# Kernel optimization log

Measured on AMD Instinct MI355X. Metric: run time of the kernel, lower is better.

## Reference

```python
import jax, jax.numpy as jnp
import numpy as np

N, E, B, D, H, C = 50000, 800000, 128, 64, 128, 2
EPS = 1e-5


def setup_inputs() -> dict:
    key = jax.random.key(0)
    ks = jax.random.split(key, 12)
    s = 0.1
    return {
        "x": jax.random.normal(ks[0], (N, D), jnp.float32),
        "edge_index": jax.random.randint(ks[1], (2, E), 0, N, jnp.int64),
        "batch": jnp.sort(jax.random.randint(ks[2], (N,), 0, B, jnp.int64)),
        "W_l": jax.random.normal(ks[3], (D, D), jnp.float32) * s,
        "b_l": jnp.zeros((D,), jnp.float32),
        "W_r": jax.random.normal(ks[4], (D, D), jnp.float32) * s,
        "W_res": jax.random.normal(ks[5], (D, D), jnp.float32) * s,
        "b_res": jnp.zeros((D,), jnp.float32),
        "gamma": jnp.ones((D,), jnp.float32),
        "beta": jnp.zeros((D,), jnp.float32),
        "gate_W1": jax.random.normal(ks[6], (D, D), jnp.float32) * s,
        "gate_b1": jnp.zeros((D,), jnp.float32),
        "gate_W2": jax.random.normal(ks[7], (D, 1), jnp.float32) * s,
        "gate_b2": jnp.zeros((1,), jnp.float32),
        "W_p1": jax.random.normal(ks[8], (D, H), jnp.float32) * s,
        "b_p1": jnp.zeros((H,), jnp.float32),
        "W_p2": jax.random.normal(ks[9], (H, C), jnp.float32) * s,
        "b_p2": jnp.zeros((C,), jnp.float32),
    }


def reference(x, edge_index, batch, W_l, b_l, W_r, W_res, b_res, gamma, beta,
              gate_W1, gate_b1, gate_W2, gate_b2, W_p1, b_p1, W_p2, b_p2):
    src, dst = edge_index[0], edge_index[1]
    # SAGEConv, mean aggregation: gather source feats, scatter-mean to target
    agg = jax.ops.segment_sum(x[src], dst, num_segments=N)          # [N, D]
    cnt = jax.ops.segment_sum(jnp.ones((E,), x.dtype), dst, num_segments=N)
    mean = agg / jnp.maximum(cnt, 1.0)[:, None]
    h = mean @ W_l + b_l + x @ W_r                                   # [N, D]
    # dropout is identity (eval mode)
    # BatchNorm1d (training-mode math: biased batch stats)
    mu = jnp.mean(h, axis=0)
    var = jnp.var(h, axis=0)
    h = (h - mu) * jax.lax.rsqrt(var + EPS) * gamma + beta
    # residual projection of the original features
    h = h + x @ W_res + b_res
    # GlobalAttention pooling: per-graph softmax over gate scores
    gate = jax.nn.relu(h @ gate_W1 + gate_b1) @ gate_W2 + gate_b2    # [N, 1]
    g = gate[:, 0]
    gmax = jax.ops.segment_max(g, batch, num_segments=B)
    gmax = jnp.where(jnp.isfinite(gmax), gmax, 0.0)
    e = jnp.exp(g - gmax[batch])
    z = jax.ops.segment_sum(e, batch, num_segments=B)
    alpha = e / jnp.maximum(z, 1e-16)[batch]
    pooled = jax.ops.segment_sum(alpha[:, None] * h, batch, num_segments=B)  # [B, D]
    # 2-layer predictor MLP with ReLU between
    out = jax.nn.relu(pooled @ W_p1 + b_p1) @ W_p2 + b_p2            # [B, C]
    return out
```

## Files before the change

kernel.cpp:

```cpp
#include <hip/hip_runtime.h>
#include <math.h>

#define N_NODES 50000
#define N_EDGES 800000
#define BATCHES 128
#define DIM 64
#define HID 128
#define NCLS 2
#define EPSV 1e-5f
#define MAXD 64

#define NPART 8
#define PART_SZ ((N_NODES + NPART - 1) / NPART)
#define EPB 2048
#define NCHK_E ((N_EDGES + EPB - 1) / EPB)
#define NCHUNK1 782

typedef __attribute__((ext_vector_type(8))) short bf16x8;
typedef __attribute__((ext_vector_type(4))) float f32x4;

__device__ __forceinline__ unsigned short f2bf(float f){
  unsigned u = __float_as_uint(f);
  u += 0x7FFFu + ((u >> 16) & 1u);
  return (unsigned short)(u >> 16);
}
__device__ __forceinline__ float bf2f(unsigned short h){
  return __uint_as_float(((unsigned)h) << 16);
}
__device__ __forceinline__ void split2(float f, unsigned short& hi, unsigned short& lo){
  hi = f2bf(f);
  lo = f2bf(f - bf2f(hi));
}
__device__ __forceinline__ uint4 pack8(const unsigned short* s){
  uint4 u;
  u.x = (unsigned)s[0] | ((unsigned)s[1] << 16);
  u.y = (unsigned)s[2] | ((unsigned)s[3] << 16);
  u.z = (unsigned)s[4] | ((unsigned)s[5] << 16);
  u.w = (unsigned)s[6] | ((unsigned)s[7] << 16);
  return u;
}

__global__ void k_scatter(const int* __restrict__ ei, int* __restrict__ cnt,
                          unsigned short* __restrict__ csr){
  const int p = blockIdx.x & (NPART-1);
  const int c = blockIdx.x >> 3;
  const int lo = p * PART_SZ;
  const int hi = lo + PART_SZ;
  const int e0 = c * EPB;
  const int e1 = (e0 + EPB < N_EDGES) ? e0 + EPB : N_EDGES;
  for (int i = e0 + threadIdx.x; i < e1; i += 256){
    int d = ei[N_EDGES + i];
    if (d >= lo && d < hi){
      int s = ei[i];
      int pos = atomicAdd(&cnt[d], 1);
      csr[(size_t)d*MAXD + pos] = (unsigned short)s;
    }
  }
}

__global__ void k_mean(const float* __restrict__ x,
                       const unsigned short* __restrict__ csr,
                       const int* __restrict__ cnt, float* __restrict__ meanb){
  const int node = (blockIdx.x*256 + threadIdx.x) >> 6;
  const int lane = threadIdx.x & 63;
  const int g = lane >> 4, f = lane & 15;
  const int dg = cnt[node];
  const size_t start = (size_t)node * MAXD;
  float4 acc = make_float4(0.f,0.f,0.f,0.f);
  int e = (lane < dg) ? (int)csr[start + lane] : 0;
  int i = 0;
  for (; i + 16 <= dg; i += 16){
    int s0 = __shfl(e, i +      g, 64);
    int s1 = __shfl(e, i + 4  + g, 64);
    int s2 = __shfl(e, i + 8  + g, 64);
    int s3 = __shfl(e, i + 12 + g, 64);
    float4 v0 = *(const float4*)&x[(size_t)s0*DIM + f*4];
    float4 v1 = *(const float4*)&x[(size_t)s1*DIM + f*4];
    float4 v2 = *(const float4*)&x[(size_t)s2*DIM + f*4];
    float4 v3 = *(const float4*)&x[(size_t)s3*DIM + f*4];
    acc.x += v0.x + v1.x + v2.x + v3.x;
    acc.y += v0.y + v1.y + v2.y + v3.y;
    acc.z += v0.z + v1.z + v2.z + v3.z;
    acc.w += v0.w + v1.w + v2.w + v3.w;
  }
  for (; i < dg; i += 4){
    int idx = i + g;
    int srcl = (idx < dg) ? idx : (dg - 1);
    int s = __shfl(e, srcl, 64);
    if (idx < dg){
      float4 v = *(const float4*)&x[(size_t)s*DIM + f*4];
      acc.x += v.x; acc.y += v.y; acc.z += v.z; acc.w += v.w;
    }
  }
  acc.x += __shfl_xor(acc.x, 16, 64); acc.x += __shfl_xor(acc.x, 32, 64);
  acc.y += __shfl_xor(acc.y, 16, 64); acc.y += __shfl_xor(acc.y, 32, 64);
  acc.z += __shfl_xor(acc.z, 16, 64); acc.z += __shfl_xor(acc.z, 32, 64);
  acc.w += __shfl_xor(acc.w, 16, 64); acc.w += __shfl_xor(acc.w, 32, 64);
  if (g == 0){
    float inv = 1.f / fmaxf((float)dg, 1.f);
    float4 r = make_float4(acc.x*inv, acc.y*inv, acc.z*inv, acc.w*inv);
    *(float4*)&meanb[(size_t)node*DIM + f*4] = r;
  }
}

__global__ void __launch_bounds__(256) k_lin1(
    const float* __restrict__ meanb, const float* __restrict__ x,
    const float* __restrict__ Wl, const float* __restrict__ bl,
    const float* __restrict__ Wr, float* __restrict__ hbuf,
    float* __restrict__ pstat){
  __shared__ __align__(16) short sB[2][64][136];
  __shared__ __align__(16) short sA[2][64][72];
  const int tid  = threadIdx.x;
  const int lane = tid & 63, w = tid >> 6;
  const int jc   = lane & 15;
  const int mrow = 16*w + jc;
  const int koff = (lane >> 4) * 8;
  const int r0   = 16*w + (lane >> 4)*4;
  const int base = blockIdx.x * 64;

  {
    const int k0 = 32 * w;
    #pragma unroll
    for (int kc = 0; kc < 4; ++kc){
      unsigned short h[8], l[8];
      #pragma unroll
      for (int i = 0; i < 8; ++i){
        int k = k0 + 8*kc + i;
        float v = (k < 64) ? Wl[k*DIM + lane] : Wr[(k-64)*DIM + lane];
        split2(v, h[i], l[i]);
      }
      *(uint4*)&sB[0][lane][k0 + 8*kc] = pack8(h);
      *(uint4*)&sB[1][lane][k0 + 8*kc] = pack8(l);
    }
  }

  float blv[4];
  #pragma unroll
  for (int nt = 0; nt < 4; ++nt) blv[nt] = bl[nt*16 + jc];

  f32x4 acc[4] = {};
  #pragma unroll
  for (int half = 0; half < 2; ++half){
    const float* __restrict__ src = half ? x : meanb;
    __syncthreads();
    {
      const int row = tid >> 2;
      const int kq  = (tid & 3) * 16;
      const int node = base + row;
      #pragma unroll
      for (int cc = 0; cc < 4; ++cc){
        float4 v = make_float4(0.f,0.f,0.f,0.f);
        if (node < N_NODES) v = *(const float4*)&src[(size_t)node*DIM + kq + 4*cc];
        unsigned short h[4], l[4];
        split2(v.x,h[0],l[0]); split2(v.y,h[1],l[1]);
        split2(v.z,h[2],l[2]); split2(v.w,h[3],l[3]);
        uint2 ph, pl;
        ph.x = (unsigned)h[0] | ((unsigned)h[1]<<16);
        ph.y = (unsigned)h[2] | ((unsigned)h[3]<<16);
        pl.x = (unsigned)l[0] | ((unsigned)l[1]<<16);
        pl.y = (unsigned)l[2] | ((unsigned)l[3]<<16);
        *(uint2*)&sA[0][row][kq + 4*cc] = ph;
        *(uint2*)&sA[1][row][kq + 4*cc] = pl;
      }
    }
    __syncthreads();
    #pragma unroll
    for (int kt2 = 0; kt2 < 2; ++kt2){
      const int ka = kt2*32 + koff;
      const int kb = half*64 + ka;
      bf16x8 ah = *(const bf16x8*)&sA[0][mrow][ka];
      bf16x8 al = *(const bf16x8*)&sA[1][mrow][ka];
      #pragma unroll
      for (int nt = 0; nt < 4; ++nt){
        const int nr = nt*16 + jc;
        bf16x8 bh = *(const bf16x8*)&sB[0][nr][kb];
        bf16x8 bo = *(const bf16x8*)&sB[1][nr][kb];
        acc[nt] = __builtin_amdgcn_mfma_f32_16x16x32_bf16(ah, bh, acc[nt], 0,0,0);
        acc[nt] = __builtin_amdgcn_mfma_f32_16x16x32_bf16(al, bh, acc[nt], 0,0,0);
        acc[nt] = __builtin_amdgcn_mfma_f32_16x16x32_bf16(ah, bo, acc[nt], 0,0,0);
      }
    }
  }

  float s1[4] = {0.f,0.f,0.f,0.f}, s2[4] = {0.f,0.f,0.f,0.f};
  #pragma unroll
  for (int nt = 0; nt < 4; ++nt){
    const int col = nt*16 + jc;
    #pragma unroll
    for (int r = 0; r < 4; ++r){
      const int node = base + r0 + r;
      float v = acc[nt][r] + blv[nt];
      if (node < N_NODES){
        hbuf[(size_t)node*DIM + col] = v;
        s1[nt] += v; s2[nt] += v*v;
      }
    }
  }

  __syncthreads();
  float* sred = (float*)sA;
  #pragma unroll
  for (int nt = 0; nt < 4; ++nt){
    float a = s1[nt], b = s2[nt];
    a += __shfl_xor(a, 16, 64); a += __shfl_xor(a, 32, 64);
    b += __shfl_xor(b, 16, 64); b += __shfl_xor(b, 32, 64);
    if ((lane >> 4) == 0){
      sred[0*256 + w*64 + nt*16 + jc] = a;
      sred[1*256 + w*64 + nt*16 + jc] = b;
    }
  }
  __syncthreads();
  if (tid < 64){
    float a = sred[tid] + sred[64+tid] + sred[128+tid] + sred[192+tid];
    float b = sred[256+tid] + sred[320+tid] + sred[384+tid] + sred[448+tid];
    pstat[(size_t)blockIdx.x*128 + tid]      = a;
    pstat[(size_t)blockIdx.x*128 + 64 + tid] = b;
  }
}

__global__ void __launch_bounds__(256) k_stats(
    const float* __restrict__ pstat, float* __restrict__ muinv){
  __shared__ float r1[256], r2[256];
  const int j = blockIdx.x;
  const int t = threadIdx.x;
  float s1 = 0.f, s2 = 0.f;
  for (int c = t; c < NCHUNK1; c += 256){
    s1 += pstat[(size_t)c*128 + j];
    s2 += pstat[(size_t)c*128 + 64 + j];
  }
  r1[t] = s1; r2[t] = s2;
  __syncthreads();
  for (int st = 128; st > 0; st >>= 1){
    if (t < st){ r1[t] += r1[t+st]; r2[t] += r2[t+st]; }
    __syncthreads();
  }
  if (t == 0){
    float mu = r1[0] / (float)N_NODES;
    float var = r2[0] / (float)N_NODES - mu*mu;
    muinv[j] = mu;
    muinv[DIM+j] = 1.0f / sqrtf(var + EPSV);
  }
}

__device__ __forceinline__ void stage_w64(short* sWh, short* sWl_,
                                          const float* __restrict__ W,
                                          int w, int lane){
  const int k0 = 16 * w;
  #pragma unroll
  for (int kc = 0; kc < 2; ++kc){
    unsigned short h[8], l[8];
    #pragma unroll
    for (int i = 0; i < 8; ++i){
      int k = k0 + 8*kc + i;
      split2(W[k*DIM + lane], h[i], l[i]);
    }
    *(uint4*)&sWh[lane*72 + k0 + 8*kc] = pack8(h);
    *(uint4*)&sWl_[lane*72 + k0 + 8*kc] = pack8(l);
  }
}

__global__ void __launch_bounds__(256) k_lin2(
    const float* __restrict__ x, const float* __restrict__ hbuf,
    const float* __restrict__ Wres, const float* __restrict__ bres,
    const float* __restrict__ gamma, const float* __restrict__ beta,
    const float* __restrict__ muinv,
    const float* __restrict__ gW1, const float* __restrict__ gb1,
    const float* __restrict__ gW2, const float* __restrict__ gb2,
    const int* __restrict__ batch,
    float* __restrict__ zbuf, float* __restrict__ pooled){
  __shared__ __align__(16) short sW[2][64][72];
  __shared__ __align__(16) short sA[2][64][72];
  __shared__ int sb[64];
  __shared__ unsigned long long runmask;
  const int tid  = threadIdx.x;
  const int lane = tid & 63, w = tid >> 6;
  const int jc   = lane & 15;
  const int g16  = w*4 + (lane >> 4);
  const int mrow = 16*w + jc;
  const int koff = (lane >> 4) * 8;
  const int r0   = 16*w + (lane >> 4)*4;
  const int base = blockIdx.x * 64;

  float muv[4], invv[4], gav[4], bev[4], brv[4], g1v[4], w2v[4];
  #pragma unroll
  for (int nt = 0; nt < 4; ++nt){
    const int col = nt*16 + jc;
    muv[nt] = muinv[col];  invv[nt] = muinv[DIM+col];
    gav[nt] = gamma[col];  bev[nt]  = beta[col];
    brv[nt] = bres[col];   g1v[nt]  = gb1[col];
    w2v[nt] = gW2[col];
  }
  const float gb2v = gb2[0];

  {
    const int row = tid >> 2;
    const int kq  = (tid & 3) * 16;
    const int node = base + row;
    #pragma unroll
    for (int cc = 0; cc < 4; ++cc){
      float4 v = make_float4(0.f,0.f,0.f,0.f);
      if (node < N_NODES) v = *(const float4*)&x[(size_t)node*DIM + kq + 4*cc];
      unsigned short h[4], l[4];
      split2(v.x,h[0],l[0]); split2(v.y,h[1],l[1]);
      split2(v.z,h[2],l[2]); split2(v.w,h[3],l[3]);
      uint2 ph, pl;
      ph.x = (unsigned)h[0] | ((unsigned)h[1]<<16);
      ph.y = (unsigned)h[2] | ((unsigned)h[3]<<16);
      pl.x = (unsigned)l[0] | ((unsigned)l[1]<<16);
      pl.y = (unsigned)l[2] | ((unsigned)l[3]<<16);
      *(uint2*)&sA[0][row][kq + 4*cc] = ph;
      *(uint2*)&sA[1][row][kq + 4*cc] = pl;
    }
  }
  if (tid < 64){
    int nn = base + tid;
    sb[tid] = batch[(nn < N_NODES) ? nn : (N_NODES-1)];
  }
  stage_w64(&sW[0][0][0], &sW[1][0][0], Wres, w, lane);
  __syncthreads();

  if (w == 0){
    bool fl = (lane > 0) && (sb[lane] != sb[lane-1]);
    unsigned long long mm = __ballot(fl);
    if (lane == 0) runmask = mm;
  }

  f32x4 acc[4] = {};
  #pragma unroll
  for (int kt2 = 0; kt2 < 2; ++kt2){
    const int ka = kt2*32 + koff;
    bf16x8 ah = *(const bf16x8*)&sA[0][mrow][ka];
    bf16x8 al = *(const bf16x8*)&sA[1][mrow][ka];
    #pragma unroll
    for (int nt = 0; nt < 4; ++nt){
      const int nr = nt*16 + jc;
      bf16x8 bh = *(const bf16x8*)&sW[0][nr][ka];
      bf16x8 bo = *(const bf16x8*)&sW[1][nr][ka];
      acc[nt] = __builtin_amdgcn_mfma_f32_16x16x32_bf16(ah, bh, acc[nt], 0,0,0);
      acc[nt] = __builtin_amdgcn_mfma_f32_16x16x32_bf16(al, bh, acc[nt], 0,0,0);
      acc[nt] = __builtin_amdgcn_mfma_f32_16x16x32_bf16(ah, bo, acc[nt], 0,0,0);
    }
  }

  float vk[4][4];
  #pragma unroll
  for (int nt = 0; nt < 4; ++nt){
    const int col = nt*16 + jc;
    #pragma unroll
    for (int r = 0; r < 4; ++r){
      const int node = base + r0 + r;
      float hp = 0.f;
      if (node < N_NODES) hp = hbuf[(size_t)node*DIM + col];
      float v = (hp - muv[nt])*invv[nt]*gav[nt] + bev[nt] + brv[nt] + acc[nt][r];
      vk[nt][r] = v;
      unsigned short hh, ll;
      split2(v, hh, ll);
      sA[0][r0 + r][col] = (short)hh;
      sA[1][r0 + r][col] = (short)ll;
    }
  }
  __syncthreads();
  stage_w64(&sW[0][0][0], &sW[1][0][0], gW1, w, lane);
  __syncthreads();

  f32x4 acc2[4] = {};
  #pragma unroll
  for (int kt2 = 0; kt2 < 2; ++kt2){
    const int ka = kt2*32 + koff;
    bf16x8 ah = *(const bf16x8*)&sA[0][mrow][ka];
    bf16x8 al = *(const bf16x8*)&sA[1][mrow][ka];
    #pragma unroll
    for (int nt = 0; nt < 4; ++nt){
      const int nr = nt*16 + jc;
      bf16x8 bh = *(const bf16x8*)&sW[0][nr][ka];
      bf16x8 bo = *(const bf16x8*)&sW[1][nr][ka];
      acc2[nt] = __builtin_amdgcn_mfma_f32_16x16x32_bf16(ah, bh, acc2[nt], 0,0,0);
      acc2[nt] = __builtin_amdgcn_mfma_f32_16x16x32_bf16(al, bh, acc2[nt], 0,0,0);
      acc2[nt] = __builtin_amdgcn_mfma_f32_16x16x32_bf16(ah, bo, acc2[nt], 0,0,0);
    }
  }

  float p[4] = {0.f,0.f,0.f,0.f};
  #pragma unroll
  for (int nt = 0; nt < 4; ++nt){
    #pragma unroll
    for (int r = 0; r < 4; ++r)
      p[r] += fmaxf(acc2[nt][r] + g1v[nt], 0.f) * w2v[nt];
  }
  float ev[4];
  #pragma unroll
  for (int r = 0; r < 4; ++r){
    float t = p[r];
    t += __shfl_xor(t, 1, 64); t += __shfl_xor(t, 2, 64);
    t += __shfl_xor(t, 4, 64); t += __shfl_xor(t, 8, 64);
    const int node = base + r0 + r;
    ev[r] = (node < N_NODES) ? expf(t + gb2v) : 0.f;
  }

  float* sredp = (float*)&sA[0][0][0];
  float* szl   = sredp + 16*64;
  __syncthreads();
  const unsigned long long m = runmask;
  int rstart = 0;
  while (rstart < 64){
    const int bseg = sb[rstart];
    unsigned long long rest = (rstart >= 63) ? 0ull : (m >> (rstart+1));
    const int rend = rest ? (rstart + 1 + __builtin_ctzll(rest)) : 64;
    float pacc[4] = {0.f,0.f,0.f,0.f};
    float zacc = 0.f;
    #pragma unroll
    for (int r = 0; r < 4; ++r){
      const int ln = 4*g16 + r;
      if (ln >= rstart && ln < rend){
        #pragma unroll
        for (int nt = 0; nt < 4; ++nt) pacc[nt] += ev[r]*vk[nt][r];
        zacc += ev[r];
      }
    }
    #pragma unroll
    for (int nt = 0; nt < 4; ++nt) sredp[g16*64 + nt*16 + jc] = pacc[nt];
    if ((lane & 15) == 0) szl[g16] = zacc;
    __syncthreads();
    if (tid < 64){
      float s = 0.f;
      #pragma unroll 4
      for (int g2 = 0; g2 < 16; ++g2) s += sredp[g2*64 + tid];
      atomicAdd(&pooled[bseg*DIM + tid], s);
    }
    if (tid == 64){
      float sz2 = 0.f;
      for (int g2 = 0; g2 < 16; ++g2) sz2 += szl[g2];
      atomicAdd(&zbuf[bseg], sz2);
    }
    __syncthreads();
    rstart = rend;
  }
}

__global__ void k_head(const float* __restrict__ pooled, const float* __restrict__ zbuf,
                       const float* __restrict__ Wp1, const float* __restrict__ bp1,
                       const float* __restrict__ Wp2, const float* __restrict__ bp2,
                       float* __restrict__ out){
  __shared__ float ps[DIM];
  __shared__ float red[4];
  int b = blockIdx.x;
  int t = threadIdx.x;
  if (t < DIM){
    float zz = fmaxf(zbuf[b], 1e-16f);
    ps[t] = pooled[b*DIM + t] / zz;
  }
  __syncthreads();
  float acc = bp1[t];
  #pragma unroll
  for (int d2=0; d2<DIM; d2++) acc = fmaf(ps[d2], Wp1[d2*HID + t], acc);
  acc = fmaxf(acc, 0.f);
  float o0 = acc * Wp2[t*NCLS+0];
  float o1 = acc * Wp2[t*NCLS+1];
  #pragma unroll
  for (int o=32;o>0;o>>=1){ o0 += __shfl_down(o0,o,64); o1 += __shfl_down(o1,o,64); }
  int w = t>>6;
  if ((t&63)==0){ red[w*2+0]=o0; red[w*2+1]=o1; }
  __syncthreads();
  if (t==0){
    out[b*NCLS+0] = red[0]+red[2]+bp2[0];
    out[b*NCLS+1] = red[1]+red[3]+bp2[1];
  }
}

extern "C" void kernel_launch(void* const* d_in, const int* in_sizes, int n_in,
                              void* d_out, int out_size, void* d_ws, size_t ws_size,
                              hipStream_t stream){
  const float* x     = (const float*)d_in[0];
  const int*   ei    = (const int*)d_in[1];
  const int*   batch = (const int*)d_in[2];
  const float* Wl    = (const float*)d_in[3];
  const float* bl    = (const float*)d_in[4];
  const float* Wr    = (const float*)d_in[5];
  const float* Wres  = (const float*)d_in[6];
  const float* bres  = (const float*)d_in[7];
  const float* gamma = (const float*)d_in[8];
  const float* beta  = (const float*)d_in[9];
  const float* gW1   = (const float*)d_in[10];
  const float* gb1   = (const float*)d_in[11];
  const float* gW2   = (const float*)d_in[12];
  const float* gb2   = (const float*)d_in[13];
  const float* Wp1   = (const float*)d_in[14];
  const float* bp1   = (const float*)d_in[15];
  const float* Wp2   = (const float*)d_in[16];
  const float* bp2   = (const float*)d_in[17];
  float* outp = (float*)d_out;

  int*   cnt   = (int*)d_ws;
  float* zbuf  = (float*)(cnt + N_NODES);
  float* pooled= zbuf + BATCHES;
  float* pstat = pooled + (size_t)BATCHES*DIM;
  float* muinv = pstat + (size_t)NCHUNK1*128;
  float* meanb = muinv + 2*DIM;
  float* hbuf  = meanb + (size_t)N_NODES*DIM;
  unsigned short* csr = (unsigned short*)(hbuf + (size_t)N_NODES*DIM);

  const size_t zcount = (size_t)N_NODES + BATCHES + (size_t)BATCHES*DIM;
  hipMemsetAsync(d_ws, 0, zcount*sizeof(int), stream);

  k_scatter<<<NPART*NCHK_E, 256, 0, stream>>>(ei, cnt, csr);
  k_mean   <<<N_NODES/4, 256, 0, stream>>>(x, csr, cnt, meanb);
  k_lin1   <<<NCHUNK1, 256, 0, stream>>>(meanb, x, Wl, bl, Wr, hbuf, pstat);
  k_stats  <<<64, 256, 0, stream>>>(pstat, muinv);
  k_lin2   <<<NCHUNK1, 256, 0, stream>>>(x, hbuf, Wres, bres, gamma, beta, muinv,
                                         gW1, gb1, gW2, gb2, batch, zbuf, pooled);
  k_head   <<<BATCHES, HID, 0, stream>>>(pooled, zbuf, Wp1, bp1, Wp2, bp2, outp);
}
```

Baseline: 200.7 us.

## Fuse lin1, stats, lin2 and head into one persistent kernel with grid barriers

Result: slower. 268.1 us (+33.6%).

```diff
diff --git a/kernel.cpp b/kernel.cpp
--- a/kernel.cpp
+++ b/kernel.cpp
@@ -14,7 +14,7 @@
 #define PART_SZ ((N_NODES + NPART - 1) / NPART)
 #define EPB 2048
 #define NCHK_E ((N_EDGES + EPB - 1) / EPB)
-#define NCHUNK1 782
+#define NBLK 391
 
 typedef __attribute__((ext_vector_type(8))) short bf16x8;
 typedef __attribute__((ext_vector_type(4))) float f32x4;
@@ -38,6 +38,24 @@
   u.z = (unsigned)s[4] | ((unsigned)s[5] << 16);
   u.w = (unsigned)s[6] | ((unsigned)s[7] << 16);
   return u;
+}
+
+__device__ __forceinline__ void gstore(float* p, float v){
+  __hip_atomic_store(p, v, __ATOMIC_RELAXED, __HIP_MEMORY_SCOPE_AGENT);
+}
+__device__ __forceinline__ float gload(const float* p){
+  return __hip_atomic_load(p, __ATOMIC_RELAXED, __HIP_MEMORY_SCOPE_AGENT);
+}
+
+__device__ __forceinline__ void gbar(unsigned* c){
+  __syncthreads();
+  if (threadIdx.x == 0){
+    __threadfence();
+    atomicAdd(c, 1u);
+    while (atomicAdd(c, 0u) < (unsigned)NBLK) __builtin_amdgcn_s_sleep(16);
+    __threadfence();
+  }
+  __syncthreads();
 }
 
 __global__ void k_scatter(const int* __restrict__ ei, int* __restrict__ cnt,
@@ -103,175 +121,195 @@
   }
 }
 
-__global__ void __launch_bounds__(256) k_lin1(
-    const float* __restrict__ meanb, const float* __restrict__ x,
-    const float* __restrict__ Wl, const float* __restrict__ bl,
-    const float* __restrict__ Wr, float* __restrict__ hbuf,
-    float* __restrict__ pstat){
-  __shared__ __align__(16) short sB[2][64][136];
-  __shared__ __align__(16) short sA[2][64][72];
-  const int tid  = threadIdx.x;
-  const int lane = tid & 63, w = tid >> 6;
-  const int jc   = lane & 15;
-  const int mrow = 16*w + jc;
-  const int koff = (lane >> 4) * 8;
-  const int r0   = 16*w + (lane >> 4)*4;
-  const int base = blockIdx.x * 64;
-
-  {
-    const int k0 = 32 * w;
-    #pragma unroll
-    for (int kc = 0; kc < 4; ++kc){
-      unsigned short h[8], l[8];
-      #pragma unroll
-      for (int i = 0; i < 8; ++i){
-        int k = k0 + 8*kc + i;
-        float v = (k < 64) ? Wl[k*DIM + lane] : Wr[(k-64)*DIM + lane];
-        split2(v, h[i], l[i]);
-      }
-      *(uint4*)&sB[0][lane][k0 + 8*kc] = pack8(h);
-      *(uint4*)&sB[1][lane][k0 + 8*kc] = pack8(l);
-    }
-  }
-
-  float blv[4];
+__device__ __forceinline__ void stage_w128(short* sBh, short* sBl,
+                                           const float* __restrict__ W0,
+                                           const float* __restrict__ W1,
+                                           int w, int lane){
+  const int k0 = 32 * w;
   #pragma unroll
-  for (int nt = 0; nt < 4; ++nt) blv[nt] = bl[nt*16 + jc];
-
-  f32x4 acc[4] = {};
-  #pragma unroll
-  for (int half = 0; half < 2; ++half){
-    const float* __restrict__ src = half ? x : meanb;
-    __syncthreads();
-    {
-      const int row = tid >> 2;
-      const int kq  = (tid & 3) * 16;
-      const int node = base + row;
-      #pragma unroll
-      for (int cc = 0; cc < 4; ++cc){
-        float4 v = make_float4(0.f,0.f,0.f,0.f);
-        if (node < N_NODES) v = *(const float4*)&src[(size_t)node*DIM + kq + 4*cc];
-        unsigned short h[4], l[4];
-        split2(v.x,h[0],l[0]); split2(v.y,h[1],l[1]);
-        split2(v.z,h[2],l[2]); split2(v.w,h[3],l[3]);
-        uint2 ph, pl;
-        ph.x = (unsigned)h[0] | ((unsigned)h[1]<<16);
-        ph.y = (unsigned)h[2] | ((unsigned)h[3]<<16);
-        pl.x = (unsigned)l[0] | ((unsigned)l[1]<<16);
-        pl.y = (unsigned)l[2] | ((unsigned)l[3]<<16);
-        *(uint2*)&sA[0][row][kq + 4*cc] = ph;
-        *(uint2*)&sA[1][row][kq + 4*cc] = pl;
-      }
-    }
-    __syncthreads();
-    #pragma unroll
-    for (int kt2 = 0; kt2 < 2; ++kt2){
-      const int ka = kt2*32 + koff;
-      const int kb = half*64 + ka;
-      bf16x8 ah = *(const bf16x8*)&sA[0][mrow][ka];
-      bf16x8 al = *(const bf16x8*)&sA[1][mrow][ka];
-      #pragma unroll
-      for (int nt = 0; nt < 4; ++nt){
-        const int nr = nt*16 + jc;
-        bf16x8 bh = *(const bf16x8*)&sB[0][nr][kb];
-        bf16x8 bo = *(const bf16x8*)&sB[1][nr][kb];
-        acc[nt] = __builtin_amdgcn_mfma_f32_16x16x32_bf16(ah, bh, acc[nt], 0,0,0);
-        acc[nt] = __builtin_amdgcn_mfma_f32_16x16x32_bf16(al, bh, acc[nt], 0,0,0);
-        acc[nt] = __builtin_amdgcn_mfma_f32_16x16x32_bf16(ah, bo, acc[nt], 0,0,0);
-      }
-    }
-  }
-
-  float s1[4] = {0.f,0.f,0.f,0.f}, s2[4] = {0.f,0.f,0.f,0.f};
-  #pragma unroll
-  for (int nt = 0; nt < 4; ++nt){
-    const int col = nt*16 + jc;
-    #pragma unroll
-    for (int r = 0; r < 4; ++r){
-      const int node = base + r0 + r;
-      float v = acc[nt][r] + blv[nt];
-      if (node < N_NODES){
-        hbuf[(size_t)node*DIM + col] = v;
-        s1[nt] += v; s2[nt] += v*v;
-      }
-    }
-  }
-
-  __syncthreads();
-  float* sred = (float*)sA;
-  #pragma unroll
-  for (int nt = 0; nt < 4; ++nt){
-    float a = s1[nt], b = s2[nt];
-    a += __shfl_xor(a, 16, 64); a += __shfl_xor(a, 32, 64);
-    b += __shfl_xor(b, 16, 64); b += __shfl_xor(b, 32, 64);
-    if ((lane >> 4) == 0){
-      sred[0*256 + w*64 + nt*16 + jc] = a;
-      sred[1*256 + w*64 + nt*16 + jc] = b;
-    }
-  }
-  __syncthreads();
-  if (tid < 64){
-    float a = sred[tid] + sred[64+tid] + sred[128+tid] + sred[192+tid];
-    float b = sred[256+tid] + sred[320+tid] + sred[384+tid] + sred[448+tid];
-    pstat[(size_t)blockIdx.x*128 + tid]      = a;
-    pstat[(size_t)blockIdx.x*128 + 64 + tid] = b;
-  }
-}
-
-__global__ void __launch_bounds__(256) k_stats(
-    const float* __restrict__ pstat, float* __restrict__ muinv){
-  __shared__ float r1[256], r2[256];
-  const int j = blockIdx.x;
-  const int t = threadIdx.x;
-  float s1 = 0.f, s2 = 0.f;
-  for (int c = t; c < NCHUNK1; c += 256){
-    s1 += pstat[(size_t)c*128 + j];
-    s2 += pstat[(size_t)c*128 + 64 + j];
-  }
-  r1[t] = s1; r2[t] = s2;
-  __syncthreads();
-  for (int st = 128; st > 0; st >>= 1){
-    if (t < st){ r1[t] += r1[t+st]; r2[t] += r2[t+st]; }
-    __syncthreads();
-  }
-  if (t == 0){
-    float mu = r1[0] / (float)N_NODES;
-    float var = r2[0] / (float)N_NODES - mu*mu;
-    muinv[j] = mu;
-    muinv[DIM+j] = 1.0f / sqrtf(var + EPSV);
-  }
-}
-
-__device__ __forceinline__ void stage_w64(short* sWh, short* sWl_,
-                                          const float* __restrict__ W,
-                                          int w, int lane){
-  const int k0 = 16 * w;
-  #pragma unroll
-  for (int kc = 0; kc < 2; ++kc){
+  for (int kc = 0; kc < 4; ++kc){
     unsigned short h[8], l[8];
     #pragma unroll
     for (int i = 0; i < 8; ++i){
       int k = k0 + 8*kc + i;
-      split2(W[k*DIM + lane], h[i], l[i]);
-    }
-    *(uint4*)&sWh[lane*72 + k0 + 8*kc] = pack8(h);
-    *(uint4*)&sWl_[lane*72 + k0 + 8*kc] = pack8(l);
-  }
-}
-
-__global__ void __launch_bounds__(256) k_lin2(
-    const float* __restrict__ x, const float* __restrict__ hbuf,
+      float v = (k < 64) ? W0[k*DIM + lane] : W1[(k-64)*DIM + lane];
+      split2(v, h[i], l[i]);
+    }
+    *(uint4*)&sBh[lane*136 + k0 + 8*kc] = pack8(h);
+    *(uint4*)&sBl[lane*136 + k0 + 8*kc] = pack8(l);
+  }
+}
+
+#define GEMM64B(SA, SB, ACC, KB0) do { \
+  _Pragma("unroll") \
+  for (int kt2 = 0; kt2 < 2; ++kt2){ \
+    const int ka = kt2*32 + koff; \
+    bf16x8 ah = *(const bf16x8*)&SA[0][mrow][ka]; \
+    bf16x8 al = *(const bf16x8*)&SA[1][mrow][ka]; \
+    _Pragma("unroll") \
+    for (int nt = 0; nt < 4; ++nt){ \
+      const int nr = nt*16 + jc; \
+      bf16x8 bh = *(const bf16x8*)&SB[0][nr][(KB0) + ka]; \
+      bf16x8 bo = *(const bf16x8*)&SB[1][nr][(KB0) + ka]; \
+      ACC[nt] = __builtin_amdgcn_mfma_f32_16x16x32_bf16(ah, bh, ACC[nt], 0,0,0); \
+      ACC[nt] = __builtin_amdgcn_mfma_f32_16x16x32_bf16(al, bh, ACC[nt], 0,0,0); \
+      ACC[nt] = __builtin_amdgcn_mfma_f32_16x16x32_bf16(ah, bo, ACC[nt], 0,0,0); \
+    } \
+  } \
+} while(0)
+
+#define STAGE_A(SRC, BASE) do { \
+  const int row_  = tid >> 2; \
+  const int kq_   = (tid & 3) * 16; \
+  const int node_ = (BASE) + row_; \
+  _Pragma("unroll") \
+  for (int cc = 0; cc < 4; ++cc){ \
+    float4 v = make_float4(0.f,0.f,0.f,0.f); \
+    if (node_ < N_NODES) v = *(const float4*)&SRC[(size_t)node_*DIM + kq_ + 4*cc]; \
+    unsigned short h_[4], l_[4]; \
+    split2(v.x,h_[0],l_[0]); split2(v.y,h_[1],l_[1]); \
+    split2(v.z,h_[2],l_[2]); split2(v.w,h_[3],l_[3]); \
+    uint2 ph_, pl_; \
+    ph_.x = (unsigned)h_[0] | ((unsigned)h_[1]<<16); \
+    ph_.y = (unsigned)h_[2] | ((unsigned)h_[3]<<16); \
+    pl_.x = (unsigned)l_[0] | ((unsigned)l_[1]<<16); \
+    pl_.y = (unsigned)l_[2] | ((unsigned)l_[3]<<16); \
+    *(uint2*)&sA[0][row_][kq_ + 4*cc] = ph_; \
+    *(uint2*)&sA[1][row_][kq_ + 4*cc] = pl_; \
+  } \
+} while(0)
+
+#define LIN1_TILE(BASE, ACC) do { \
+  STAGE_A(meanb, BASE); \
+  __syncthreads(); \
+  GEMM64B(sA, sB, ACC, 0); \
+  __syncthreads(); \
+  STAGE_A(x, BASE); \
+  __syncthreads(); \
+  GEMM64B(sA, sB, ACC, 64); \
+  __syncthreads(); \
+} while(0)
+
+#define EPI1(BASE, ACC) do { \
+  _Pragma("unroll") \
+  for (int nt = 0; nt < 4; ++nt){ \
+    _Pragma("unroll") \
+    for (int r = 0; r < 4; ++r){ \
+      const int node_ = (BASE) + r0 + r; \
+      float v_ = ACC[nt][r] + blv[nt]; \
+      ACC[nt][r] = v_; \
+      if (node_ < N_NODES){ s1v[nt] += v_; s2v[nt] += v_*v_; } \
+    } \
+  } \
+} while(0)
+
+#define LIN2_TILE(BASE, ACC) do { \
+  if (tid < 64){ \
+    int nn_ = (BASE) + tid; \
+    sb[tid] = batch[(nn_ < N_NODES) ? nn_ : (N_NODES-1)]; \
+  } \
+  STAGE_A(x, BASE); \
+  __syncthreads(); \
+  if (w == 0){ \
+    bool fl_ = (lane > 0) && (sb[lane] != sb[lane-1]); \
+    unsigned long long mm_ = __ballot(fl_); \
+    if (lane == 0) runmask = mm_; \
+  } \
+  f32x4 acc2_[4] = {}; \
+  GEMM64B(sA, sB, acc2_, 0); \
+  _Pragma("unroll") \
+  for (int nt = 0; nt < 4; ++nt){ \
+    const int col_ = nt*16 + jc; \
+    _Pragma("unroll") \
+    for (int r = 0; r < 4; ++r){ \
+      float v_ = (ACC[nt][r] - muv[nt])*invv[nt]*gav[nt] + bev[nt] \
+               + brv[nt] + acc2_[nt][r]; \
+      ACC[nt][r] = v_; \
+      unsigned short hh_, ll_; \
+      split2(v_, hh_, ll_); \
+      sA[0][r0 + r][col_] = (short)hh_; \
+      sA[1][r0 + r][col_] = (short)ll_; \
+    } \
+  } \
+  __syncthreads(); \
+  f32x4 acc3_[4] = {}; \
+  GEMM64B(sA, sB, acc3_, 64); \
+  float p_[4] = {0.f,0.f,0.f,0.f}; \
+  _Pragma("unroll") \
+  for (int nt = 0; nt < 4; ++nt){ \
+    _Pragma("unroll") \
+    for (int r = 0; r < 4; ++r) \
+      p_[r] += fmaxf(acc3_[nt][r] + g1v[nt], 0.f) * w2v[nt]; \
+  } \
+  float ev_[4]; \
+  _Pragma("unroll") \
+  for (int r = 0; r < 4; ++r){ \
+    float t_ = p_[r]; \
+    t_ += __shfl_xor(t_, 1, 64); t_ += __shfl_xor(t_, 2, 64); \
+    t_ += __shfl_xor(t_, 4, 64); t_ += __shfl_xor(t_, 8, 64); \
+    const int node_ = (BASE) + r0 + r; \
+    ev_[r] = (node_ < N_NODES) ? expf(t_ + gb2v) : 0.f; \
+  } \
+  float* sredp_ = (float*)&sA[0][0][0]; \
+  float* szl_   = sredp_ + 16*64; \
+  __syncthreads(); \
+  const unsigned long long m_ = runmask; \
+  int rstart_ = 0; \
+  while (rstart_ < 64){ \
+    const int bseg_ = sb[rstart_]; \
+    unsigned long long rest_ = (rstart_ >= 63) ? 0ull : (m_ >> (rstart_+1)); \
+    const int rend_ = rest_ ? (rstart_ + 1 + __builtin_ctzll(rest_)) : 64; \
+    float pacc_[4] = {0.f,0.f,0.f,0.f}; \
+    float zacc_ = 0.f; \
+    _Pragma("unroll") \
+    for (int r = 0; r < 4; ++r){ \
+      const int ln_ = 4*g16 + r; \
+      if (ln_ >= rstart_ && ln_ < rend_){ \
+        _Pragma("unroll") \
+        for (int nt = 0; nt < 4; ++nt) pacc_[nt] += ev_[r]*ACC[nt][r]; \
+        zacc_ += ev_[r]; \
+      } \
+    } \
+    _Pragma("unroll") \
+    for (int nt = 0; nt < 4; ++nt) sredp_[g16*64 + nt*16 + jc] = pacc_[nt]; \
+    if ((lane & 15) == 0) szl_[g16] = zacc_; \
+    __syncthreads(); \
+    if (tid < 64){ \
+      float s_ = 0.f; \
+      for (int g2 = 0; g2 < 16; ++g2) s_ += sredp_[g2*64 + tid]; \
+      atomicAdd(&pooled[bseg_*DIM + tid], s_); \
+    } \
+    if (tid == 64){ \
+      float sz2_ = 0.f; \
+      for (int g2 = 0; g2 < 16; ++g2) sz2_ += szl_[g2]; \
+      atomicAdd(&zbuf[bseg_], sz2_); \
+    } \
+    __syncthreads(); \
+    rstart_ = rend_; \
+  } \
+} while(0)
+
+__global__ void __launch_bounds__(256, 2) k_mega(
+    const float* __restrict__ meanb, const float* __restrict__ x,
+    const float* __restrict__ Wl, const float* __restrict__ bl,
+    const float* __restrict__ Wr,
     const float* __restrict__ Wres, const float* __restrict__ bres,
     const float* __restrict__ gamma, const float* __restrict__ beta,
-    const float* __restrict__ muinv,
     const float* __restrict__ gW1, const float* __restrict__ gb1,
     const float* __restrict__ gW2, const float* __restrict__ gb2,
+    const float* __restrict__ Wp1, const float* __restrict__ bp1,
+    const float* __restrict__ Wp2, const float* __restrict__ bp2,
     const int* __restrict__ batch,
-    float* __restrict__ zbuf, float* __restrict__ pooled){
-  __shared__ __align__(16) short sW[2][64][72];
+    float* __restrict__ pstat, float* __restrict__ muinv,
+    float* __restrict__ zbuf, float* __restrict__ pooled,
+    unsigned* __restrict__ bar, float* __restrict__ outp){
   __shared__ __align__(16) short sA[2][64][72];
+  __shared__ __align__(16) short sB[2][64][136];
   __shared__ int sb[64];
   __shared__ unsigned long long runmask;
+  __shared__ float psh[DIM];
+  __shared__ float redh[4];
+
   const int tid  = threadIdx.x;
   const int lane = tid & 63, w = tid >> 6;
   const int jc   = lane & 15;
@@ -279,191 +317,111 @@
   const int mrow = 16*w + jc;
   const int koff = (lane >> 4) * 8;
   const int r0   = 16*w + (lane >> 4)*4;
-  const int base = blockIdx.x * 64;
+  const int bx   = blockIdx.x;
+  const int baseA = (2*bx) * 64;
+  const int baseB = (2*bx + 1) * 64;
+
+  float blv[4];
+  #pragma unroll
+  for (int nt = 0; nt < 4; ++nt) blv[nt] = bl[nt*16 + jc];
+  stage_w128(&sB[0][0][0], &sB[1][0][0], Wl, Wr, w, lane);
+
+  f32x4 accA[4] = {};
+  f32x4 accB[4] = {};
+  LIN1_TILE(baseA, accA);
+  LIN1_TILE(baseB, accB);
+
+  float s1v[4] = {0.f,0.f,0.f,0.f}, s2v[4] = {0.f,0.f,0.f,0.f};
+  EPI1(baseA, accA);
+  EPI1(baseB, accB);
+  {
+    float* sred = (float*)&sA[0][0][0];
+    #pragma unroll
+    for (int nt = 0; nt < 4; ++nt){
+      float a = s1v[nt], b = s2v[nt];
+      a += __shfl_xor(a, 16, 64); a += __shfl_xor(a, 32, 64);
+      b += __shfl_xor(b, 16, 64); b += __shfl_xor(b, 32, 64);
+      if ((lane >> 4) == 0){
+        sred[0*256 + w*64 + nt*16 + jc] = a;
+        sred[1*256 + w*64 + nt*16 + jc] = b;
+      }
+    }
+    __syncthreads();
+    if (tid < 64){
+      float a = sred[tid] + sred[64+tid] + sred[128+tid] + sred[192+tid];
+      float b = sred[256+tid] + sred[320+tid] + sred[384+tid] + sred[448+tid];
+      gstore(&pstat[(size_t)bx*128 + tid], a);
+      gstore(&pstat[(size_t)bx*128 + 64 + tid], b);
+    }
+  }
+  gbar(&bar[0]);
+
+  if (bx < 64){
+    float* r1 = (float*)&sA[0][0][0];
+    float* r2 = r1 + 256;
+    float s1 = 0.f, s2 = 0.f;
+    for (int c = tid; c < NBLK; c += 256){
+      s1 += gload(&pstat[(size_t)c*128 + bx]);
+      s2 += gload(&pstat[(size_t)c*128 + 64 + bx]);
+    }
+    r1[tid] = s1; r2[tid] = s2;
+    __syncthreads();
+    for (int st = 128; st > 0; st >>= 1){
+      if (tid < st){ r1[tid] += r1[tid+st]; r2[tid] += r2[tid+st]; }
+      __syncthreads();
+    }
+    if (tid == 0){
+      float mu = r1[0] / (float)N_NODES;
+      float var = r2[0] / (float)N_NODES - mu*mu;
+      gstore(&muinv[bx], mu);
+      gstore(&muinv[DIM+bx], 1.0f / sqrtf(var + EPSV));
+    }
+  }
+  gbar(&bar[1]);
 
   float muv[4], invv[4], gav[4], bev[4], brv[4], g1v[4], w2v[4];
   #pragma unroll
   for (int nt = 0; nt < 4; ++nt){
     const int col = nt*16 + jc;
-    muv[nt] = muinv[col];  invv[nt] = muinv[DIM+col];
-    gav[nt] = gamma[col];  bev[nt]  = beta[col];
-    brv[nt] = bres[col];   g1v[nt]  = gb1[col];
+    muv[nt] = gload(&muinv[col]);  invv[nt] = gload(&muinv[DIM+col]);
+    gav[nt] = gamma[col];   bev[nt] = beta[col];
+    brv[nt] = bres[col];    g1v[nt] = gb1[col];
     w2v[nt] = gW2[col];
   }
   const float gb2v = gb2[0];
-
-  {
-    const int row = tid >> 2;
-    const int kq  = (tid & 3) * 16;
-    const int node = base + row;
-    #pragma unroll
-    for (int cc = 0; cc < 4; ++cc){
-      float4 v = make_float4(0.f,0.f,0.f,0.f);
-      if (node < N_NODES) v = *(const float4*)&x[(size_t)node*DIM + kq + 4*cc];
-      unsigned short h[4], l[4];
-      split2(v.x,h[0],l[0]); split2(v.y,h[1],l[1]);
-      split2(v.z,h[2],l[2]); split2(v.w,h[3],l[3]);
-      uint2 ph, pl;
-      ph.x = (unsigned)h[0] | ((unsigned)h[1]<<16);
-      ph.y = (unsigned)h[2] | ((unsigned)h[3]<<16);
-      pl.x = (unsigned)l[0] | ((unsigned)l[1]<<16);
-      pl.y = (unsigned)l[2] | ((unsigned)l[3]<<16);
-      *(uint2*)&sA[0][row][kq + 4*cc] = ph;
-      *(uint2*)&sA[1][row][kq + 4*cc] = pl;
-    }
-  }
-  if (tid < 64){
-    int nn = base + tid;
-    sb[tid] = batch[(nn < N_NODES) ? nn : (N_NODES-1)];
-  }
-  stage_w64(&sW[0][0][0], &sW[1][0][0], Wres, w, lane);
-  __syncthreads();
-
-  if (w == 0){
-    bool fl = (lane > 0) && (sb[lane] != sb[lane-1]);
-    unsigned long long mm = __ballot(fl);
-    if (lane == 0) runmask = mm;
-  }
-
-  f32x4 acc[4] = {};
-  #pragma unroll
-  for (int kt2 = 0; kt2 < 2; ++kt2){
-    const int ka = kt2*32 + koff;
-    bf16x8 ah = *(const bf16x8*)&sA[0][mrow][ka];
-    bf16x8 al = *(const bf16x8*)&sA[1][mrow][ka];
-    #pragma unroll
-    for (int nt = 0; nt < 4; ++nt){
-      const int nr = nt*16 + jc;
-      bf16x8 bh = *(const bf16x8*)&sW[0][nr][ka];
-      bf16x8 bo = *(const bf16x8*)&sW[1][nr][ka];
-      acc[nt] = __builtin_amdgcn_mfma_f32_16x16x32_bf16(ah, bh, acc[nt], 0,0,0);
-      acc[nt] = __builtin_amdgcn_mfma_f32_16x16x32_bf16(al, bh, acc[nt], 0,0,0);
-      acc[nt] = __builtin_amdgcn_mfma_f32_16x16x32_bf16(ah, bo, acc[nt], 0,0,0);
-    }
-  }
-
-  float vk[4][4];
-  #pragma unroll
-  for (int nt = 0; nt < 4; ++nt){
-    const int col = nt*16 + jc;
-    #pragma unroll
-    for (int r = 0; r < 4; ++r){
-      const int node = base + r0 + r;
-      float hp = 0.f;
-      if (node < N_NODES) hp = hbuf[(size_t)node*DIM + col];
-      float v = (hp - muv[nt])*invv[nt]*gav[nt] + bev[nt] + brv[nt] + acc[nt][r];
-      vk[nt][r] = v;
-      unsigned short hh, ll;
-      split2(v, hh, ll);
-      sA[0][r0 + r][col] = (short)hh;
-      sA[1][r0 + r][col] = (short)ll;
-    }
-  }
-  __syncthreads();
-  stage_w64(&sW[0][0][0], &sW[1][0][0], gW1, w, lane);
-  __syncthreads();
-
-  f32x4 acc2[4] = {};
-  #pragma unroll
-  for (int kt2 = 0; kt2 < 2; ++kt2){
-    const int ka = kt2*32 + koff;
-    bf16x8 ah = *(const bf16x8*)&sA[0][mrow][ka];
-    bf16x8 al = *(const bf16x8*)&sA[1][mrow][ka];
-    #pragma unroll
-    for (int nt = 0; nt < 4; ++nt){
-      const int nr = nt*16 + jc;
-      bf16x8 bh = *(const bf16x8*)&sW[0][nr][ka];
-      bf16x8 bo = *(const bf16x8*)&sW[1][nr][ka];
-      acc2[nt] = __builtin_amdgcn_mfma_f32_16x16x32_bf16(ah, bh, acc2[nt], 0,0,0);
-      acc2[nt] = __builtin_amdgcn_mfma_f32_16x16x32_bf16(al, bh, acc2[nt], 0,0,0);
-      acc2[nt] = __builtin_amdgcn_mfma_f32_16x16x32_bf16(ah, bo, acc2[nt], 0,0,0);
-    }
-  }
-
-  float p[4] = {0.f,0.f,0.f,0.f};
-  #pragma unroll
-  for (int nt = 0; nt < 4; ++nt){
-    #pragma unroll
-    for (int r = 0; r < 4; ++r)
-      p[r] += fmaxf(acc2[nt][r] + g1v[nt], 0.f) * w2v[nt];
-  }
-  float ev[4];
-  #pragma unroll
-  for (int r = 0; r < 4; ++r){
-    float t = p[r];
-    t += __shfl_xor(t, 1, 64); t += __shfl_xor(t, 2, 64);
-    t += __shfl_xor(t, 4, 64); t += __shfl_xor(t, 8, 64);
-    const int node = base + r0 + r;
-    ev[r] = (node < N_NODES) ? expf(t + gb2v) : 0.f;
-  }
-
-  float* sredp = (float*)&sA[0][0][0];
-  float* szl   = sredp + 16*64;
-  __syncthreads();
-  const unsigned long long m = runmask;
-  int rstart = 0;
-  while (rstart < 64){
-    const int bseg = sb[rstart];
-    unsigned long long rest = (rstart >= 63) ? 0ull : (m >> (rstart+1));
-    const int rend = rest ? (rstart + 1 + __builtin_ctzll(rest)) : 64;
-    float pacc[4] = {0.f,0.f,0.f,0.f};
-    float zacc = 0.f;
-    #pragma unroll
-    for (int r = 0; r < 4; ++r){
-      const int ln = 4*g16 + r;
-      if (ln >= rstart && ln < rend){
-        #pragma unroll
-        for (int nt = 0; nt < 4; ++nt) pacc[nt] += ev[r]*vk[nt][r];
-        zacc += ev[r];
+  stage_w128(&sB[0][0][0], &sB[1][0][0], Wres, gW1, w, lane);
+
+  LIN2_TILE(baseA, accA);
+  LIN2_TILE(baseB, accB);
+  gbar(&bar[2]);
+
+  if (bx < BATCHES){
+    const int b = bx;
+    const int t = tid;
+    if (t < DIM){
+      float zz = fmaxf(gload(&zbuf[b]), 1e-16f);
+      psh[t] = gload(&pooled[b*DIM + t]) / zz;
+    }
+    __syncthreads();
+    if (t < HID){
+      float a = bp1[t];
+      #pragma unroll
+      for (int d2 = 0; d2 < DIM; ++d2) a = fmaf(psh[d2], Wp1[d2*HID + t], a);
+      a = fmaxf(a, 0.f);
+      float o0 = a * Wp2[t*NCLS+0];
+      float o1 = a * Wp2[t*NCLS+1];
+      #pragma unroll
+      for (int o = 32; o > 0; o >>= 1){
+        o0 += __shfl_down(o0, o, 64); o1 += __shfl_down(o1, o, 64);
       }
-    }
-    #pragma unroll
-    for (int nt = 0; nt < 4; ++nt) sredp[g16*64 + nt*16 + jc] = pacc[nt];
-    if ((lane & 15) == 0) szl[g16] = zacc;
+      int hw = t >> 6;
+      if ((t & 63) == 0){ redh[hw*2+0] = o0; redh[hw*2+1] = o1; }
+    }
     __syncthreads();
-    if (tid < 64){
-      float s = 0.f;
-      #pragma unroll 4
-      for (int g2 = 0; g2 < 16; ++g2) s += sredp[g2*64 + tid];
-      atomicAdd(&pooled[bseg*DIM + tid], s);
-    }
-    if (tid == 64){
-      float sz2 = 0.f;
-      for (int g2 = 0; g2 < 16; ++g2) sz2 += szl[g2];
-      atomicAdd(&zbuf[bseg], sz2);
-    }
-    __syncthreads();
-    rstart = rend;
-  }
-}
-
-__global__ void k_head(const float* __restrict__ pooled, const float* __restrict__ zbuf,
-                       const float* __restrict__ Wp1, const float* __restrict__ bp1,
-                       const float* __restrict__ Wp2, const float* __restrict__ bp2,
-                       float* __restrict__ out){
-  __shared__ float ps[DIM];
-  __shared__ float red[4];
-  int b = blockIdx.x;
-  int t = threadIdx.x;
-  if (t < DIM){
-    float zz = fmaxf(zbuf[b], 1e-16f);
-    ps[t] = pooled[b*DIM + t] / zz;
-  }
-  __syncthreads();
-  float acc = bp1[t];
-  #pragma unroll
-  for (int d2=0; d2<DIM; d2++) acc = fmaf(ps[d2], Wp1[d2*HID + t], acc);
-  acc = fmaxf(acc, 0.f);
-  float o0 = acc * Wp2[t*NCLS+0];
-  float o1 = acc * Wp2[t*NCLS+1];
-  #pragma unroll
-  for (int o=32;o>0;o>>=1){ o0 += __shfl_down(o0,o,64); o1 += __shfl_down(o1,o,64); }
-  int w = t>>6;
-  if ((t&63)==0){ red[w*2+0]=o0; red[w*2+1]=o1; }
-  __syncthreads();
-  if (t==0){
-    out[b*NCLS+0] = red[0]+red[2]+bp2[0];
-    out[b*NCLS+1] = red[1]+red[3]+bp2[1];
+    if (t == 0){
+      outp[b*NCLS+0] = redh[0]+redh[2]+bp2[0];
+      outp[b*NCLS+1] = redh[1]+redh[3]+bp2[1];
+    }
   }
 }
 
@@ -490,23 +448,22 @@
   const float* bp2   = (const float*)d_in[17];
   float* outp = (float*)d_out;
 
-  int*   cnt   = (int*)d_ws;
-  float* zbuf  = (float*)(cnt + N_NODES);
-  float* pooled= zbuf + BATCHES;
-  float* pstat = pooled + (size_t)BATCHES*DIM;
-  float* muinv = pstat + (size_t)NCHUNK1*128;
-  float* meanb = muinv + 2*DIM;
-  float* hbuf  = meanb + (size_t)N_NODES*DIM;
-  unsigned short* csr = (unsigned short*)(hbuf + (size_t)N_NODES*DIM);
-
-  const size_t zcount = (size_t)N_NODES + BATCHES + (size_t)BATCHES*DIM;
+  int*      cnt    = (int*)d_ws;
+  float*    zbuf   = (float*)(cnt + N_NODES);
+  float*    pooled = zbuf + BATCHES;
+  unsigned* bar    = (unsigned*)(pooled + (size_t)BATCHES*DIM);
+  float*    pstat  = (float*)(bar + 8);
+  float*    muinv  = pstat + (size_t)NBLK*128;
+  float*    meanb  = muinv + 2*DIM;
+  unsigned short* csr = (unsigned short*)(meanb + (size_t)N_NODES*DIM);
+
+  const size_t zcount = (size_t)N_NODES + BATCHES + (size_t)BATCHES*DIM + 8;
   hipMemsetAsync(d_ws, 0, zcount*sizeof(int), stream);
 
   k_scatter<<<NPART*NCHK_E, 256, 0, stream>>>(ei, cnt, csr);
   k_mean   <<<N_NODES/4, 256, 0, stream>>>(x, csr, cnt, meanb);
-  k_lin1   <<<NCHUNK1, 256, 0, stream>>>(meanb, x, Wl, bl, Wr, hbuf, pstat);
-  k_stats  <<<64, 256, 0, stream>>>(pstat, muinv);
-  k_lin2   <<<NCHUNK1, 256, 0, stream>>>(x, hbuf, Wres, bres, gamma, beta, muinv,
-                                         gW1, gb1, gW2, gb2, batch, zbuf, pooled);
-  k_head   <<<BATCHES, HID, 0, stream>>>(pooled, zbuf, Wp1, bp1, Wp2, bp2, outp);
-}
+  k_mega   <<<NBLK, 256, 0, stream>>>(meanb, x, Wl, bl, Wr, Wres, bres,
+                                      gamma, beta, gW1, gb1, gW2, gb2,
+                                      Wp1, bp1, Wp2, bp2, batch,
+                                      pstat, muinv, zbuf, pooled, bar, outp);
+}
```
